# Kernel optimization log

Measured on AMD Instinct MI355X. Metric: run time of the kernel, lower is better.

Reference implementation:

```python
import jax, jax.numpy as jnp
import numpy as np

TEMPERATURE = 0.3
BASE_TEMPERATURE = 0.07
EPS = 1e-08


def setup_inputs() -> dict:
    key = jax.random.key(0)
    k1, k2 = jax.random.split(key)
    bsz, n_views, f_dim = 4096, 2, 128
    features = jax.random.normal(k1, (bsz, n_views, f_dim), dtype=jnp.float32)
    # L2-normalize as is standard for contrastive features (keeps logits well-scaled)
    features = features / jnp.linalg.norm(features, axis=-1, keepdims=True)
    labels = jax.random.randint(k2, (bsz,), 0, 2, dtype=jnp.int64)
    return {"features": features, "labels": labels}


def reference(features, labels):
    # features: [B, V, D], labels: [B]
    B, V, D = features.shape
    N = B * V

    # mask[i,j] = 1 if labels[i] == labels[j]
    mask = (labels[:, None] == labels[None, :]).astype(jnp.float32)  # [B, B]

    # torch.cat(torch.unbind(features, dim=1), dim=0): view-major stacking -> [V*B, D]
    contrast_feature = features.transpose(1, 0, 2).reshape(N, D)
    anchor_feature = contrast_feature  # contrast_mode == 'all'

    logits = jnp.matmul(anchor_feature, contrast_feature.T) / TEMPERATURE  # [N, N]
    logits = logits - jax.lax.stop_gradient(jnp.max(logits, axis=1, keepdims=True))

    mask = jnp.tile(mask, (V, V))  # [N, N]
    logits_mask = 1.0 - jnp.eye(N, dtype=jnp.float32)  # mask out self-contrast
    mask = mask * logits_mask

    exp_logits = jnp.exp(logits) * logits_mask
    log_prob = logits - jnp.log(jnp.sum(exp_logits, axis=1, keepdims=True) + EPS)

    mean_log_prob_pos = jnp.sum(mask * log_prob, axis=1) / (jnp.sum(mask, axis=1) + EPS)
    loss = -(TEMPERATURE / BASE_TEMPERATURE) * mean_log_prob_pos  # [N]
    return jnp.mean(loss.reshape(V, B))
```

## Files before the change

### kernel.cpp

```cpp
#include <hip/hip_runtime.h>
#include <hip/hip_bf16.h>

constexpr int B_SZ  = 4096;
constexpr int N_SZ  = 8192;
constexpr int CHUNK = 512;
constexpr int TILE  = 64;
constexpr int NT    = CHUNK / TILE;
constexpr int NCH   = N_SZ / CHUNK;
constexpr int BROWS = 128;

typedef __attribute__((ext_vector_type(8))) __bf16 bf16x8;
typedef __attribute__((ext_vector_type(4))) float f32x4;

#define SQRT_CSC  2.1929404f
#define SELF_EXP  28.0316248f
#define NEG_RATIO (-(0.3f / 0.07f))

__device__ __forceinline__ unsigned short f2bf(float f) {
    unsigned u = __float_as_uint(f);
    u += 0x7FFFu + ((u >> 16) & 1u);
    return (unsigned short)(u >> 16);
}

__device__ __forceinline__ void gl_lds16(const unsigned short* g, unsigned short* l) {
    __builtin_amdgcn_global_load_lds(
        (const __attribute__((address_space(1))) unsigned int*)g,
        (__attribute__((address_space(3))) unsigned int*)l, 16, 0, 0);
}

__global__ __launch_bounds__(256) void prep_kernel(const float* __restrict__ feat,
                                                   unsigned short* __restrict__ A,
                                                   float* __restrict__ out) {
    const int tid = threadIdx.x;
    if (blockIdx.x == 0 && tid == 0) out[0] = 0.f;
    int t = blockIdx.x * 256 + tid;
    int n = t >> 5;
    int q = (t & 31) << 2;
    int b = n & (B_SZ - 1);
    int v = n >> 12;
    const float4 f = *reinterpret_cast<const float4*>(feat + (((size_t)b * 2 + v) << 7) + q);
    ushort4 o;
    o.x = f2bf(f.x * SQRT_CSC); o.y = f2bf(f.y * SQRT_CSC);
    o.z = f2bf(f.z * SQRT_CSC); o.w = f2bf(f.w * SQRT_CSC);
    *reinterpret_cast<ushort4*>(A + (((size_t)n) << 7) + q) = o;
}

__global__ __launch_bounds__(256) void msum_kernel(const float* __restrict__ feat,
                                                   const int* __restrict__ labels,
                                                   float* __restrict__ mpart) {
    __shared__ float sm[2][256];
    const int tid = threadIdx.x;
    const int v = tid >> 7, d = tid & 127;
    const int b0 = blockIdx.x * 16;
    float a0 = 0.f, a1 = 0.f;
#pragma unroll
    for (int it = 0; it < 16; ++it) {
        const int b = b0 + it;
        const float x = feat[(((size_t)b * 2 + v) << 7) + d];
        if (labels[b]) a1 += x; else a0 += x;
    }
    sm[0][tid] = a0; sm[1][tid] = a1;
    __syncthreads();
    if (tid < 128)
        mpart[(size_t)tid * 256 + blockIdx.x] = sm[0][tid] + sm[0][tid + 128];
    else
        mpart[(size_t)tid * 256 + blockIdx.x] = sm[1][tid - 128] + sm[1][tid];
}

__global__ __launch_bounds__(256, 2) void gram_kernel(const unsigned short* __restrict__ A,
                                                      float* __restrict__ S_part) {
    __shared__ __align__(16) unsigned short tb[2][TILE * 128];

    const int tid  = threadIdx.x;
    const int wave = tid >> 6;
    const int lane = tid & 63;
    const int grp  = lane >> 4;
    const int lc   = lane & 15;
    const int row0 = blockIdx.x * BROWS + wave * 32;
    const int col0 = blockIdx.y * CHUNK;

    bf16x8 a[2][4];
#pragma unroll
    for (int rt = 0; rt < 2; ++rt) {
        const unsigned short* ap = A + ((size_t)(row0 + 16 * rt + lc) << 7) + grp * 8;
#pragma unroll
        for (int g = 0; g < 4; ++g)
            a[rt][g] = *reinterpret_cast<const bf16x8*>(ap + g * 32);
    }

    int off[4];
#pragma unroll
    for (int g = 0; g < 4; ++g)
        off[g] = lc * 128 + (((4 * g + grp) ^ (lc & 7)) << 3);

    float s_acc[2][4] = {{0,0,0,0},{0,0,0,0}};

    auto stage = [&](int buf, int tt) {
        const unsigned short* gbase = A + ((size_t)(col0 + tt * TILE) << 7);
#pragma unroll
        for (int k = 0; k < 4; ++k) {
            const int s = tid + 256 * k;
            const int r = s >> 4, c = s & 15;
            const int src = (r << 4) + (c ^ (r & 7));
            gl_lds16(gbase + src * 8, &tb[buf][s * 8]);
        }
    };

    stage(0, 0);
    __syncthreads();

#pragma clang loop unroll(disable)
    for (int t = 0; t < NT; ++t) {
        const int cur = t & 1;
        if (t + 1 < NT) stage(cur ^ 1, t + 1);

        const unsigned short* bp = &tb[cur][0];
#pragma unroll
        for (int ct = 0; ct < 4; ++ct) {
            bf16x8 bfr[4];
#pragma unroll
            for (int g = 0; g < 4; ++g)
                bfr[g] = *reinterpret_cast<const bf16x8*>(bp + ct * 2048 + off[g]);

            f32x4 acc0 = {0,0,0,0}, acc1 = {0,0,0,0};
#pragma unroll
            for (int g = 0; g < 4; ++g) {
                acc0 = __builtin_amdgcn_mfma_f32_16x16x32_bf16(a[0][g], bfr[g], acc0, 0, 0, 0);
                acc1 = __builtin_amdgcn_mfma_f32_16x16x32_bf16(a[1][g], bfr[g], acc1, 0, 0, 0);
            }
#pragma unroll
            for (int r = 0; r < 4; ++r) {
                s_acc[0][r] += __builtin_amdgcn_exp2f(acc0[r]);
                s_acc[1][r] += __builtin_amdgcn_exp2f(acc1[r]);
            }
        }
        __syncthreads();
    }

#pragma unroll
    for (int m = 1; m < 16; m <<= 1)
#pragma unroll
        for (int rt = 0; rt < 2; ++rt)
#pragma unroll
            for (int r = 0; r < 4; ++r)
                s_acc[rt][r] += __shfl_xor(s_acc[rt][r], m);

    if (lc == 0) {
        const size_t base = (size_t)blockIdx.y * N_SZ;
#pragma unroll
        for (int rt = 0; rt < 2; ++rt)
#pragma unroll
            for (int r = 0; r < 4; ++r)
                S_part[base + row0 + 16 * rt + 4 * grp + r] = s_acc[rt][r];
    }
}

__global__ __launch_bounds__(256) void final_kernel(const float* __restrict__ S_part,
                                                    const float* __restrict__ feat,
                                                    const int* __restrict__ labels,
                                                    const float* __restrict__ mpart,
                                                    float* __restrict__ out) {
    __shared__ float mv[256];
    __shared__ float red[4];
    __shared__ int   redi[4];
    const int tid = threadIdx.x;

    {
        const float* p = mpart + (size_t)tid * 256;
        float s = 0.f;
#pragma unroll 8
        for (int k = 0; k < 256; k += 4) {
            const float4 x = *reinterpret_cast<const float4*>(p + k);
            s += x.x + x.y + x.z + x.w;
        }
        mv[tid] = s;
    }

    int c = 0;
    for (int i = tid; i < B_SZ; i += 256) c += labels[i];
#pragma unroll
    for (int m = 1; m < 64; m <<= 1) c += __shfl_xor(c, m);
    if ((tid & 63) == 0) redi[tid >> 6] = c;
    __syncthreads();
    const int c1 = redi[0] + redi[1] + redi[2] + redi[3];

    const int i = blockIdx.x * 256 + tid;
    float S = -SELF_EXP;
#pragma unroll
    for (int k = 0; k < NCH; ++k) S += S_part[(size_t)k * N_SZ + i];

    const int b = i & (B_SZ - 1), v = i >> 12;
    const int lab = labels[b];
    const float* fr = feat + (((size_t)b * 2 + v) << 7);
    const float* mvp = &mv[lab ? 128 : 0];
    float dot = 0.f;
#pragma unroll 8
    for (int d = 0; d < 128; d += 4) {
        const float4 x = *reinterpret_cast<const float4*>(fr + d);
        dot += x.x * mvp[d] + x.y * mvp[d + 1] + x.z * mvp[d + 2] + x.w * mvp[d + 3];
    }

    const int cs = lab ? c1 : (B_SZ - c1);
    const float n = (float)(2 * cs - 1);
    float term = ((dot - 1.0f) * (1.0f / 0.3f) - n * logf(S + 1e-8f)) / (n + 1e-8f);

#pragma unroll
    for (int m = 1; m < 64; m <<= 1) term += __shfl_xor(term, m);
    if ((tid & 63) == 0) red[tid >> 6] = term;
    __syncthreads();
    if (tid == 0)
        atomicAdd(out, (red[0] + red[1] + red[2] + red[3]) * (NEG_RATIO / (float)N_SZ));
}

extern "C" void kernel_launch(void* const* d_in, const int* in_sizes, int n_in,
                              void* d_out, int out_size, void* d_ws, size_t ws_size,
                              hipStream_t stream) {
    const float* feat = (const float*)d_in[0];
    const int* labels = (const int*)d_in[1];
    float* out = (float*)d_out;

    char* ws = (char*)d_ws;
    unsigned short* A = (unsigned short*)ws;
    float* S_part = (float*)(ws + (size_t)2 * 1024 * 1024);
    float* mpart  = (float*)(ws + (size_t)2 * 1024 * 1024 + 512 * 1024);

    prep_kernel<<<dim3(1024), dim3(256), 0, stream>>>(feat, A, out);
    msum_kernel<<<dim3(256), dim3(256), 0, stream>>>(feat, labels, mpart);
    gram_kernel<<<dim3(N_SZ / BROWS, NCH), dim3(256), 0, stream>>>(A, S_part);
    final_kernel<<<dim3(N_SZ / 256), dim3(256), 0, stream>>>(S_part, feat, labels, mpart, out);
}
```

Measured before the change: 47.42 us.

## Shrink gram tiles, raise occupancy, and precompute LDS staging pointers

Halves the column chunk and LDS tile size in the gram kernel, which doubles the grid along columns, and raises the launch-bounds minimum blocks per CU from 2 to 3. The staging lambda is replaced with precomputed source and destination pointers plus XOR-toggled buffer offsets, and B fragments are loaded per MFMA instead of batched, to cut address arithmetic and register pressure. The aim is more resident waves and a smaller LDS footprint to hide load latency. The trade-off is twice as many partial sums for the final reduction and less compute per block against each sync. The workspace offset for mpart is moved to make room for the larger S_part.

```diff
diff --git a/kernel.cpp b/kernel.cpp
--- a/kernel.cpp
+++ b/kernel.cpp
@@ -3,8 +3,8 @@
 
 constexpr int B_SZ  = 4096;
 constexpr int N_SZ  = 8192;
-constexpr int CHUNK = 512;
-constexpr int TILE  = 64;
+constexpr int CHUNK = 256;
+constexpr int TILE  = 32;
 constexpr int NT    = CHUNK / TILE;
 constexpr int NCH   = N_SZ / CHUNK;
 constexpr int BROWS = 128;
@@ -67,7 +67,7 @@
         mpart[(size_t)tid * 256 + blockIdx.x] = sm[1][tid - 128] + sm[1][tid];
 }
 
-__global__ __launch_bounds__(256, 2) void gram_kernel(const unsigned short* __restrict__ A,
+__global__ __launch_bounds__(256, 3) void gram_kernel(const unsigned short* __restrict__ A,
                                                       float* __restrict__ S_part) {
     __shared__ __align__(16) unsigned short tb[2][TILE * 128];
 
@@ -88,45 +88,46 @@
             a[rt][g] = *reinterpret_cast<const bf16x8*>(ap + g * 32);
     }
 
-    int off[4];
+    const char* tb0 = (const char*)&tb[0][0];
+    const char* bq[4];
 #pragma unroll
     for (int g = 0; g < 4; ++g)
-        off[g] = lc * 128 + (((4 * g + grp) ^ (lc & 7)) << 3);
+        bq[g] = tb0 + lc * 256 + ((((4 * g + grp) ^ (lc & 7))) << 4);
+
+    const int s1 = tid + 256;
+    const int r0s = tid >> 4,  c0s = tid & 15;
+    const int r1s = s1 >> 4,   c1s = s1 & 15;
+    const unsigned short* src0 = A + ((size_t)(col0 + r0s) << 7) + ((c0s ^ (r0s & 7)) << 3);
+    const unsigned short* src1 = A + ((size_t)(col0 + r1s) << 7) + ((c1s ^ (r1s & 7)) << 3);
+    unsigned short* d0 = &tb[0][0] + tid * 8;
+    unsigned short* d1 = d0 + 2048;
 
     float s_acc[2][4] = {{0,0,0,0},{0,0,0,0}};
 
-    auto stage = [&](int buf, int tt) {
-        const unsigned short* gbase = A + ((size_t)(col0 + tt * TILE) << 7);
-#pragma unroll
-        for (int k = 0; k < 4; ++k) {
-            const int s = tid + 256 * k;
-            const int r = s >> 4, c = s & 15;
-            const int src = (r << 4) + (c ^ (r & 7));
-            gl_lds16(gbase + src * 8, &tb[buf][s * 8]);
-        }
-    };
-
-    stage(0, 0);
-    __syncthreads();
+    gl_lds16(src0, d0);
+    gl_lds16(src1, d1);
+    src0 += TILE * 128; src1 += TILE * 128;
+    __syncthreads();
+
+    int ro = 0;
+    int so = 8192;
 
 #pragma clang loop unroll(disable)
     for (int t = 0; t < NT; ++t) {
-        const int cur = t & 1;
-        if (t + 1 < NT) stage(cur ^ 1, t + 1);
-
-        const unsigned short* bp = &tb[cur][0];
-#pragma unroll
-        for (int ct = 0; ct < 4; ++ct) {
-            bf16x8 bfr[4];
-#pragma unroll
-            for (int g = 0; g < 4; ++g)
-                bfr[g] = *reinterpret_cast<const bf16x8*>(bp + ct * 2048 + off[g]);
-
+        if (t + 1 < NT) {
+            gl_lds16(src0, (unsigned short*)((char*)d0 + so));
+            gl_lds16(src1, (unsigned short*)((char*)d1 + so));
+            src0 += TILE * 128; src1 += TILE * 128;
+        }
+
+#pragma unroll
+        for (int ct = 0; ct < 2; ++ct) {
             f32x4 acc0 = {0,0,0,0}, acc1 = {0,0,0,0};
 #pragma unroll
             for (int g = 0; g < 4; ++g) {
-                acc0 = __builtin_amdgcn_mfma_f32_16x16x32_bf16(a[0][g], bfr[g], acc0, 0, 0, 0);
-                acc1 = __builtin_amdgcn_mfma_f32_16x16x32_bf16(a[1][g], bfr[g], acc1, 0, 0, 0);
+                const bf16x8 bfr = *reinterpret_cast<const bf16x8*>(bq[g] + ro + ct * 4096);
+                acc0 = __builtin_amdgcn_mfma_f32_16x16x32_bf16(a[0][g], bfr, acc0, 0, 0, 0);
+                acc1 = __builtin_amdgcn_mfma_f32_16x16x32_bf16(a[1][g], bfr, acc1, 0, 0, 0);
             }
 #pragma unroll
             for (int r = 0; r < 4; ++r) {
@@ -135,6 +136,7 @@
             }
         }
         __syncthreads();
+        ro ^= 8192; so ^= 8192;
     }
 
 #pragma unroll
@@ -222,7 +224,7 @@
     char* ws = (char*)d_ws;
     unsigned short* A = (unsigned short*)ws;
     float* S_part = (float*)(ws + (size_t)2 * 1024 * 1024);
-    float* mpart  = (float*)(ws + (size_t)2 * 1024 * 1024 + 512 * 1024);
+    float* mpart  = (float*)(ws + (size_t)3 * 1024 * 1024);
 
     prep_kernel<<<dim3(1024), dim3(256), 0, stream>>>(feat, A, out);
     msum_kernel<<<dim3(256), dim3(256), 0, stream>>>(feat, labels, mpart);
```

Measured after the change: 49.49 us. 1.04x slower.
